# Kernel tuning notes

Hardware: AMD Instinct MI355X
Metric: run time of the kernel (lower is better)

The kernel has to match this reference:

```python
import jax, jax.numpy as jnp
import numpy as np
import math

B, S, E, H, L, C, DFF = 8, 1024, 512, 8, 2, 8921, 2048
DH = E // H
LN_EPS = 1e-5


def _make_pe(max_len, d):
    pos = np.arange(max_len, dtype=np.float32)[:, None]
    div = np.exp(np.arange(0, d, 2, dtype=np.float32) * (-math.log(10000.0) / d))
    pe = np.zeros((max_len, d), dtype=np.float32)
    pe[:, 0::2] = np.sin(pos * div)
    pe[:, 1::2] = np.cos(pos * div)
    return jnp.asarray(pe)


def setup_inputs() -> dict:
    key = jax.random.key(0)
    ks = jax.random.split(key, 16)
    sc = 0.02
    return {
        'inputs': jax.random.normal(ks[0], (B, S, E), jnp.float32),
        'pe': _make_pe(S, E),
        'label_mat': jax.random.normal(ks[1], (C, E), jnp.float32) * sc,
        'l1_w': jax.random.normal(ks[2], (E, E), jnp.float32) * sc,
        'l1_b': jnp.zeros((E,), jnp.float32),
        'fc_w': jax.random.normal(ks[3], (C, E), jnp.float32) * sc,
        'fc_b': jnp.zeros((C,), jnp.float32),
        'in_proj_w': jax.random.normal(ks[4], (L, 3 * E, E), jnp.float32) * sc,
        'in_proj_b': jnp.zeros((L, 3 * E), jnp.float32),
        'out_proj_w': jax.random.normal(ks[5], (L, E, E), jnp.float32) * sc,
        'out_proj_b': jnp.zeros((L, E), jnp.float32),
        'ln1_w': jnp.ones((L, E), jnp.float32),
        'ln1_b': jnp.zeros((L, E), jnp.float32),
        'ln2_w': jnp.ones((L, E), jnp.float32),
        'ln2_b': jnp.zeros((L, E), jnp.float32),
        'lin1_w': jax.random.normal(ks[6], (L, DFF, E), jnp.float32) * sc,
        'lin1_b': jnp.zeros((L, DFF), jnp.float32),
        'lin2_w': jax.random.normal(ks[7], (L, E, DFF), jnp.float32) * sc,
        'lin2_b': jnp.zeros((L, E), jnp.float32),
    }


def _ln(x, g, b):
    mu = jnp.mean(x, axis=-1, keepdims=True)
    v = jnp.mean(jnp.square(x - mu), axis=-1, keepdims=True)
    return (x - mu) * jax.lax.rsqrt(v + LN_EPS) * g + b


def _encoder_layer(x, wqkv, bqkv, wo, bo, g1, b1, g2, b2, w1, bb1, w2, bb2):
    # x: [B,S,E]; post-norm torch TransformerEncoderLayer with relu
    qkv = x @ wqkv.T + bqkv                      # [B,S,3E]
    q, k, v = jnp.split(qkv, 3, axis=-1)
    q = q.reshape(B, S, H, DH)
    k = k.reshape(B, S, H, DH)
    v = v.reshape(B, S, H, DH)
    scores = jnp.einsum('bqhd,bkhd->bhqk', q, k) / math.sqrt(DH)
    attn = jax.nn.softmax(scores, axis=-1)
    o = jnp.einsum('bhqk,bkhd->bqhd', attn, v).reshape(B, S, E)
    o = o @ wo.T + bo
    x = _ln(x + o, g1, b1)
    ff = jax.nn.relu(x @ w1.T + bb1) @ w2.T + bb2
    return _ln(x + ff, g2, b2)


def reference(inputs, pe, label_mat, l1_w, l1_b, fc_w, fc_b,
              in_proj_w, in_proj_b, out_proj_w, out_proj_b,
              ln1_w, ln1_b, ln2_w, ln2_b,
              lin1_w, lin1_b, lin2_w, lin2_b):
    # faithful to source: pe is indexed by batch position (source bug)
    x = inputs * math.sqrt(E) + pe[:B][:, None, :]      # [B,S,E]
    for i in range(L):
        x = _encoder_layer(x, in_proj_w[i], in_proj_b[i], out_proj_w[i], out_proj_b[i],
                           ln1_w[i], ln1_b[i], ln2_w[i], ln2_b[i],
                           lin1_w[i], lin1_b[i], lin2_w[i], lin2_b[i])
    # label attention
    o1 = jnp.tanh(x @ l1_w.T + l1_b)                    # [B,S,E]
    scores = o1 @ label_mat.T                           # [B,S,C]
    attn_weights = jax.nn.softmax(scores, axis=1)       # over seq dim
    attn_weights = jnp.swapaxes(attn_weights, 1, 2)     # [B,C,S]
    weighted = attn_weights @ x                         # [B,C,E]
    # fused per-class linears: C tiny GEMVs -> one einsum
    outputs = jnp.einsum('bce,ce->bc', weighted, fc_w) + fc_b  # [B,C]
    return outputs, attn_weights
```

## Files before the change

### kernel.cpp

```cpp
#include <hip/hip_runtime.h>
#include <math.h>

#define BB   8
#define SS   1024
#define EE   512
#define HH   8
#define DHH  64
#define LLY  2
#define CC   8921
#define CP   9088
#define DFF_ 2048

typedef short          bf16x8 __attribute__((ext_vector_type(8)));
typedef float          f32x4  __attribute__((ext_vector_type(4)));
typedef unsigned short u16x4  __attribute__((ext_vector_type(4)));
typedef unsigned short u16x8  __attribute__((ext_vector_type(8)));

__device__ __forceinline__ float bf2f(unsigned short u) {
    return __uint_as_float(((unsigned int)u) << 16);
}
__device__ __forceinline__ unsigned short f2bf(float f) {
    unsigned int u = __float_as_uint(f);
    u = (u + 0x7FFFu + ((u >> 16) & 1u)) >> 16;
    return (unsigned short)u;
}
__device__ __forceinline__ void gload16(const void* g, void* l) {
    __builtin_amdgcn_global_load_lds(
        (const __attribute__((address_space(1))) void*)g,
        (__attribute__((address_space(3))) void*)l, 16, 0, 0);
}

__global__ __launch_bounds__(256) void cvt_bf16(const float* __restrict__ in,
                                                unsigned short* __restrict__ out,
                                                long n_in, long n_out)
{
    const long i4 = ((long)blockIdx.x * 256 + threadIdx.x) * 4;
    if (i4 >= n_out) return;
    u16x4 r;
    if (i4 < n_in) {
        const float4 v = *(const float4*)(in + i4);
        r[0] = f2bf(v.x); r[1] = f2bf(v.y); r[2] = f2bf(v.z); r[3] = f2bf(v.w);
    } else {
        r[0] = r[1] = r[2] = r[3] = 0;
    }
    *(u16x4*)(out + i4) = r;
}

__global__ __launch_bounds__(256) void embed_kernel(const float* __restrict__ in,
                                                    const float* __restrict__ pe,
                                                    float* __restrict__ x,
                                                    unsigned short* __restrict__ xb)
{
    const long i  = (long)blockIdx.x * 256 + threadIdx.x;
    const int  e4 = (int)(i & 127);
    const int  b  = (int)(i >> 17);
    float4 v = ((const float4*)in)[i];
    const float4 p = ((const float4*)pe)[b * 128 + e4];
    const float sc = 22.627416997969522f;
    v.x = v.x * sc + p.x;  v.y = v.y * sc + p.y;
    v.z = v.z * sc + p.z;  v.w = v.w * sc + p.w;
    ((float4*)x)[i] = v;
    u16x4 h; h[0] = f2bf(v.x); h[1] = f2bf(v.y); h[2] = f2bf(v.z); h[3] = f2bf(v.w);
    ((u16x4*)xb)[i] = h;
}

__global__ __launch_bounds__(256) void gemm_mfma(const unsigned short* __restrict__ A,
                                                 const unsigned short* __restrict__ B,
                                                 const float* __restrict__ bias,
                                                 float* __restrict__ Cf,
                                                 unsigned short* __restrict__ Ch,
                                                 int M, int N, int K, int Mlim,
                                                 long sAz, long sBz, long sCz,
                                                 int act, int mode)
{
    __shared__ unsigned short As[128 * 64];
    __shared__ unsigned short Bs[128 * 64];
    const int t  = threadIdx.x;
    const int wv = t >> 6, ln = t & 63;
    const int wr = wv >> 1, wc = wv & 1;
    const int lr = ln & 15, lg = ln >> 4;
    const int m0 = blockIdx.x * 128, n0 = blockIdx.y * 128;
    const int z  = blockIdx.z;
    const unsigned short* Ab = A + (long)z * sAz;
    const unsigned short* Bb = B + (long)z * sBz;

    const int srow = ln >> 3;
    const int ucol = ((ln & 7) ^ srow) << 3;

    f32x4 acc[4][4];
    #pragma unroll
    for (int i = 0; i < 4; ++i)
        #pragma unroll
        for (int j = 0; j < 4; ++j)
            acc[i][j] = (f32x4){0.f, 0.f, 0.f, 0.f};

    int rA[4], rB[4];
    #pragma unroll
    for (int f = 0; f < 4; ++f) {
        rA[f] = wr * 64 + f * 16 + lr;
        rB[f] = wc * 64 + f * 16 + lr;
    }

    for (int k0 = 0; k0 < K; k0 += 64) {
        __syncthreads();
        #pragma unroll
        for (int c = 0; c < 4; ++c) {
            const int q   = (wv << 2) + c;
            const int row = (q << 3) + srow;
            gload16(Ab + (long)(m0 + row) * K + k0 + ucol, (char*)As + (q << 10));
            gload16(Bb + (long)(n0 + row) * K + k0 + ucol, (char*)Bs + (q << 10));
        }
        __syncthreads();
        #pragma unroll
        for (int kk = 0; kk < 2; ++kk) {
            bf16x8 af[4], bg[4];
            const int s = (kk << 2) + lg;
            #pragma unroll
            for (int f = 0; f < 4; ++f) {
                af[f] = *(const bf16x8*)((const char*)As + rA[f] * 128 + ((s ^ (rA[f] & 7)) << 4));
                bg[f] = *(const bf16x8*)((const char*)Bs + rB[f] * 128 + ((s ^ (rB[f] & 7)) << 4));
            }
            #pragma unroll
            for (int i = 0; i < 4; ++i)
                #pragma unroll
                for (int j = 0; j < 4; ++j)
                    acc[i][j] = __builtin_amdgcn_mfma_f32_16x16x32_bf16(af[i], bg[j], acc[i][j], 0, 0, 0);
        }
    }

    const long zC = (long)z * sCz;
    #pragma unroll
    for (int fm = 0; fm < 4; ++fm) {
        #pragma unroll
        for (int reg = 0; reg < 4; ++reg) {
            const int gm = m0 + wr * 64 + fm * 16 + lg * 4 + reg;
            if (gm >= Mlim) continue;
            #pragma unroll
            for (int fn = 0; fn < 4; ++fn) {
                const int gn = n0 + wc * 64 + fn * 16 + lr;
                float v = acc[fm][fn][reg];
                if (bias) v += bias[gn];
                if (act == 1)      v = fmaxf(v, 0.f);
                else if (act == 2) v = tanhf(v);
                if (mode & 1) Cf[zC + (long)gm * N + gn] = v;
                if (mode & 2) Ch[zC + (long)gm * N + gn] = f2bf(v);
            }
        }
    }
}

__global__ __launch_bounds__(256) void gemm_label_mfma(const unsigned short* __restrict__ A,
                                                       const unsigned short* __restrict__ B,
                                                       const float* __restrict__ attn,
                                                       float* __restrict__ out)
{
    __shared__ unsigned short As[128 * 64];
    __shared__ unsigned short Bs[128 * 64];
    const int t  = threadIdx.x;
    const int wv = t >> 6, ln = t & 63;
    const int wr = wv >> 1, wc = wv & 1;
    const int lr = ln & 15, lg = ln >> 4;
    const int m0 = blockIdx.x * 128, n0 = blockIdx.y * 128;
    const int z  = blockIdx.z;
    const unsigned short* Bb = B + (long)z * SS * EE;

    const int srow = ln >> 3;
    const int ucol = ((ln & 7) ^ srow) << 3;

    f32x4 acc[4][4];
    #pragma unroll
    for (int i = 0; i < 4; ++i)
        #pragma unroll
        for (int j = 0; j < 4; ++j)
            acc[i][j] = (f32x4){0.f, 0.f, 0.f, 0.f};

    int rA[4], rB[4];
    #pragma unroll
    for (int f = 0; f < 4; ++f) {
        rA[f] = wr * 64 + f * 16 + lr;
        rB[f] = wc * 64 + f * 16 + lr;
    }

    for (int k0 = 0; k0 < EE; k0 += 64) {
        __syncthreads();
        #pragma unroll
        for (int c = 0; c < 4; ++c) {
            const int q   = (wv << 2) + c;
            const int row = (q << 3) + srow;
            gload16(A  + (long)(m0 + row) * EE + k0 + ucol, (char*)As + (q << 10));
            gload16(Bb + (long)(n0 + row) * EE + k0 + ucol, (char*)Bs + (q << 10));
        }
        __syncthreads();
        #pragma unroll
        for (int kk = 0; kk < 2; ++kk) {
            bf16x8 af[4], bg[4];
            const int s = (kk << 2) + lg;
            #pragma unroll
            for (int f = 0; f < 4; ++f) {
                af[f] = *(const bf16x8*)((const char*)As + rA[f] * 128 + ((s ^ (rA[f] & 7)) << 4));
                bg[f] = *(const bf16x8*)((const char*)Bs + rB[f] * 128 + ((s ^ (rB[f] & 7)) << 4));
            }
            #pragma unroll
            for (int i = 0; i < 4; ++i)
                #pragma unroll
                for (int j = 0; j < 4; ++j)
                    acc[i][j] = __builtin_amdgcn_mfma_f32_16x16x32_bf16(af[i], bg[j], acc[i][j], 0, 0, 0);
        }
    }

    const float* attb = attn + (long)z * CC * SS;
    float*       outb = out  + (long)z * CC;
    #pragma unroll
    for (int fm = 0; fm < 4; ++fm) {
        #pragma unroll
        for (int reg = 0; reg < 4; ++reg) {
            const int r = m0 + wr * 64 + fm * 16 + lg * 4 + reg;
            float p = 0.f;
            if (r < CC) {
                #pragma unroll
                for (int fn = 0; fn < 4; ++fn) {
                    const int sn = n0 + wc * 64 + fn * 16 + lr;
                    p += acc[fm][fn][reg] * attb[(long)r * SS + sn];
                }
            }
            p += __shfl_xor(p, 1);
            p += __shfl_xor(p, 2);
            p += __shfl_xor(p, 4);
            p += __shfl_xor(p, 8);
            if (lr == 0 && r < CC) atomicAdd(&outb[r], p);
        }
    }
}

__global__ __launch_bounds__(256) void vtrans(const unsigned short* __restrict__ qkv,
                                              unsigned short* __restrict__ Vt)
{
    __shared__ unsigned short tile[64][72];
    const int bh = blockIdx.y, b = bh >> 3, h = bh & 7;
    const int s0 = blockIdx.x << 6;
    const int t  = threadIdx.x;
    const int r  = t >> 3;
    const int c8 = (t & 7) << 3;
    const unsigned short* vb = qkv + (long)b * SS * 1536 + 2 * EE + h * DHH;
    #pragma unroll
    for (int rr = 0; rr < 64; rr += 32)
        *(u16x8*)&tile[r + rr][c8] = *(const u16x8*)(vb + (long)(s0 + r + rr) * 1536 + c8);
    __syncthreads();
    #pragma unroll
    for (int rr = 0; rr < 64; rr += 32) {
        const int d = r + rr;
        u16x8 o;
        #pragma unroll
        for (int j = 0; j < 8; ++j) o[j] = tile[c8 + j][d];
        *(u16x8*)(Vt + ((long)bh * DHH + d) * SS + s0 + c8) = o;
    }
}

__global__ __launch_bounds__(256) void flash_mfma(const unsigned short* __restrict__ qkv,
                                                  const unsigned short* __restrict__ Vt,
                                                  unsigned short* __restrict__ o)
{
    __shared__ unsigned short sP[4][16 * 64];
    const int t  = threadIdx.x;
    const int wv = t >> 6, ln = t & 63;
    const int lr = ln & 15, lg = ln >> 4;
    const int bh = blockIdx.y, b = bh >> 3, h = bh & 7;
    const int q0 = (blockIdx.x << 6) + (wv << 4);

    const unsigned short* qb = qkv + (long)b * SS * 1536 + h * DHH;
    const unsigned short* kb = qb + EE;
    const unsigned short* vt = Vt + (long)bh * DHH * SS;
    unsigned short* pw = sP[wv];

    bf16x8 aq[2];
    #pragma unroll
    for (int c = 0; c < 2; ++c)
        aq[c] = *(const bf16x8*)(qb + (long)(q0 + lr) * 1536 + (c << 5) + (lg << 3));

    float m_[4], l_[4];
    f32x4 accO[4];
    #pragma unroll
    for (int r = 0; r < 4; ++r) { m_[r] = -1e30f; l_[r] = 0.f; }
    #pragma unroll
    for (int n = 0; n < 4; ++n) accO[n] = (f32x4){0.f, 0.f, 0.f, 0.f};

    for (int s0 = 0; s0 < SS; s0 += 64) {
        f32x4 accS[4];
        #pragma unroll
        for (int sj = 0; sj < 4; ++sj) accS[sj] = (f32x4){0.f, 0.f, 0.f, 0.f};
        #pragma unroll
        for (int c = 0; c < 2; ++c) {
            #pragma unroll
            for (int sj = 0; sj < 4; ++sj) {
                const bf16x8 kf = *(const bf16x8*)(kb + (long)(s0 + (sj << 4) + lr) * 1536 + (c << 5) + (lg << 3));
                accS[sj] = __builtin_amdgcn_mfma_f32_16x16x32_bf16(aq[c], kf, accS[sj], 0, 0, 0);
            }
        }
        #pragma unroll
        for (int reg = 0; reg < 4; ++reg) {
            float sc0 = accS[0][reg] * 0.125f, sc1 = accS[1][reg] * 0.125f;
            float sc2 = accS[2][reg] * 0.125f, sc3 = accS[3][reg] * 0.125f;
            float mx = fmaxf(fmaxf(sc0, sc1), fmaxf(sc2, sc3));
            mx = fmaxf(mx, __shfl_xor(mx, 1));
            mx = fmaxf(mx, __shfl_xor(mx, 2));
            mx = fmaxf(mx, __shfl_xor(mx, 4));
            mx = fmaxf(mx, __shfl_xor(mx, 8));
            const float mnew = fmaxf(m_[reg], mx);
            const float f = __expf(m_[reg] - mnew);
            m_[reg] = mnew;
            sc0 = __expf(sc0 - mnew); sc1 = __expf(sc1 - mnew);
            sc2 = __expf(sc2 - mnew); sc3 = __expf(sc3 - mnew);
            accS[0][reg] = sc0; accS[1][reg] = sc1;
            accS[2][reg] = sc2; accS[3][reg] = sc3;
            float ss = sc0 + sc1 + sc2 + sc3;
            ss += __shfl_xor(ss, 1); ss += __shfl_xor(ss, 2);
            ss += __shfl_xor(ss, 4); ss += __shfl_xor(ss, 8);
            l_[reg] = l_[reg] * f + ss;
            #pragma unroll
            for (int n = 0; n < 4; ++n) accO[n][reg] *= f;
        }
        #pragma unroll
        for (int sj = 0; sj < 4; ++sj) {
            #pragma unroll
            for (int reg = 0; reg < 4; ++reg) {
                const int q = (lg << 2) + reg;
                const int s = (sj << 4) + lr;
                const int byte = (q << 7) + (((s >> 3) ^ (q & 7)) << 4) + ((s & 7) << 1);
                *(unsigned short*)((char*)pw + byte) = f2bf(accS[sj][reg]);
            }
        }
        #pragma unroll
        for (int c2 = 0; c2 < 2; ++c2) {
            const int slot = ((c2 << 2) + lg) ^ (lr & 7);
            const bf16x8 pa = *(const bf16x8*)((const char*)pw + (lr << 7) + (slot << 4));
            #pragma unroll
            for (int n = 0; n < 4; ++n) {
                const bf16x8 vf = *(const bf16x8*)(vt + (long)((n << 4) + lr) * SS + s0 + (c2 << 5) + (lg << 3));
                accO[n] = __builtin_amdgcn_mfma_f32_16x16x32_bf16(pa, vf, accO[n], 0, 0, 0);
            }
        }
    }

    #pragma unroll
    for (int reg = 0; reg < 4; ++reg) {
        const float inv = 1.f / l_[reg];
        unsigned short* orow = o + (long)(b * SS + q0 + (lg << 2) + reg) * EE + h * DHH;
        #pragma unroll
        for (int n = 0; n < 4; ++n)
            orow[(n << 4) + lr] = f2bf(accO[n][reg] * inv);
    }
}

__global__ __launch_bounds__(256) void ln_fused(float* __restrict__ x,
                                                unsigned short* __restrict__ xb,
                                                const float* __restrict__ o,
                                                const float* __restrict__ g,
                                                const float* __restrict__ bta)
{
    const long row = blockIdx.x;
    float* xr = x + row * EE;
    unsigned short* hb = xb + row * EE;
    const float* orr = o + row * EE;
    const int t = threadIdx.x;
    const float v0 = xr[t] + orr[t];
    const float v1 = xr[t + 256] + orr[t + 256];
    float s = v0 + v1;
    #pragma unroll
    for (int off = 1; off < 64; off <<= 1) s += __shfl_xor(s, off);
    __shared__ float r1[4], r2[4];
    if ((t & 63) == 0) r1[t >> 6] = s;
    __syncthreads();
    const float mu = (r1[0] + r1[1] + r1[2] + r1[3]) * (1.f / EE);
    const float d0 = v0 - mu, d1 = v1 - mu;
    float q = d0 * d0 + d1 * d1;
    #pragma unroll
    for (int off = 1; off < 64; off <<= 1) q += __shfl_xor(q, off);
    if ((t & 63) == 0) r2[t >> 6] = q;
    __syncthreads();
    const float rs = rsqrtf((r2[0] + r2[1] + r2[2] + r2[3]) * (1.f / EE) + 1e-5f);
    const float y0 = d0 * rs * g[t]       + bta[t];
    const float y1 = d1 * rs * g[t + 256] + bta[t + 256];
    xr[t] = y0;  xr[t + 256] = y1;
    hb[t] = f2bf(y0);  hb[t + 256] = f2bf(y1);
}

__global__ __launch_bounds__(256) void label_softmax(float* __restrict__ attn)
{
    const long row = blockIdx.x;
    float* p = attn + row * (long)SS;
    const int t = threadIdx.x;
    float4 v = ((float4*)p)[t];
    __shared__ float red[4];
    float mx = fmaxf(fmaxf(v.x, v.y), fmaxf(v.z, v.w));
    #pragma unroll
    for (int off = 1; off < 64; off <<= 1) mx = fmaxf(mx, __shfl_xor(mx, off));
    if ((t & 63) == 0) red[t >> 6] = mx;
    __syncthreads();
    mx = fmaxf(fmaxf(red[0], red[1]), fmaxf(red[2], red[3]));
    v.x = __expf(v.x - mx); v.y = __expf(v.y - mx);
    v.z = __expf(v.z - mx); v.w = __expf(v.w - mx);
    float s = v.x + v.y + v.z + v.w;
    #pragma unroll
    for (int off = 1; off < 64; off <<= 1) s += __shfl_xor(s, off);
    __syncthreads();
    if ((t & 63) == 0) red[t >> 6] = s;
    __syncthreads();
    const float inv = 1.f / (red[0] + red[1] + red[2] + red[3]);
    v.x *= inv; v.y *= inv; v.z *= inv; v.w *= inv;
    ((float4*)p)[t] = v;
}

__global__ __launch_bounds__(256) void init_out(float* __restrict__ out,
                                                const float* __restrict__ fcb)
{
    const int i = blockIdx.x * 256 + threadIdx.x;
    if (i < BB * CC) out[i] = fcb[i % CC];
}

extern "C" void kernel_launch(void* const* d_in, const int* in_sizes, int n_in,
                              void* d_out, int out_size, void* d_ws, size_t ws_size,
                              hipStream_t stream)
{
    const float* inp   = (const float*)d_in[0];
    const float* pe    = (const float*)d_in[1];
    const float* label = (const float*)d_in[2];
    const float* l1w   = (const float*)d_in[3];
    const float* l1b   = (const float*)d_in[4];
    const float* fcw   = (const float*)d_in[5];
    const float* fcb   = (const float*)d_in[6];
    const float* ipw   = (const float*)d_in[7];
    const float* ipb   = (const float*)d_in[8];
    const float* opw   = (const float*)d_in[9];
    const float* opb   = (const float*)d_in[10];
    const float* g1    = (const float*)d_in[11];
    const float* b1    = (const float*)d_in[12];
    const float* g2    = (const float*)d_in[13];
    const float* b2    = (const float*)d_in[14];
    const float* w1    = (const float*)d_in[15];
    const float* bb1   = (const float*)d_in[16];
    const float* w2    = (const float*)d_in[17];
    const float* bb2   = (const float*)d_in[18];

    char* wp = (char*)d_ws;
    float* x = (float*)wp;                 wp += (long)BB * SS * EE * 4;
    unsigned short* xb = (unsigned short*)wp;  wp += (long)BB * SS * EE * 2;
    float* bufo = (float*)wp;              wp += (long)BB * SS * EE * 4;
    unsigned short* big = (unsigned short*)wp; wp += (long)BB * SS * DFF_ * 2;
    unsigned short* ob  = (unsigned short*)wp; wp += (long)BB * SS * EE * 2;
    unsigned short* Vtb = (unsigned short*)wp; wp += (long)BB * HH * DHH * SS * 2;
    unsigned short* ipwb = (unsigned short*)wp; wp += (long)LLY * 3 * EE * EE * 2;
    unsigned short* opwb = (unsigned short*)wp; wp += (long)LLY * EE * EE * 2;
    unsigned short* w1b  = (unsigned short*)wp; wp += (long)LLY * DFF_ * EE * 2;
    unsigned short* w2b  = (unsigned short*)wp; wp += (long)LLY * EE * DFF_ * 2;
    unsigned short* l1wb = (unsigned short*)wp; wp += (long)EE * EE * 2;
    unsigned short* labelb = (unsigned short*)wp; wp += (long)CP * EE * 2;
    unsigned short* fcwb   = (unsigned short*)wp; wp += (long)CP * EE * 2;

    float* out0  = (float*)d_out;
    float* attnW = out0 + BB * CC;

    {
        const long n1 = (long)LLY * 3 * EE * EE;
        cvt_bf16<<<(int)((n1 / 4 + 255) / 256), 256, 0, stream>>>(ipw, ipwb, n1, n1);
        const long n2 = (long)LLY * EE * EE;
        cvt_bf16<<<(int)((n2 / 4 + 255) / 256), 256, 0, stream>>>(opw, opwb, n2, n2);
        const long n3 = (long)LLY * DFF_ * EE;
        cvt_bf16<<<(int)((n3 / 4 + 255) / 256), 256, 0, stream>>>(w1, w1b, n3, n3);
        cvt_bf16<<<(int)((n3 / 4 + 255) / 256), 256, 0, stream>>>(w2, w2b, n3, n3);
        const long n4 = (long)EE * EE;
        cvt_bf16<<<(int)((n4 / 4 + 255) / 256), 256, 0, stream>>>(l1w, l1wb, n4, n4);
        const long n5i = (long)CC * EE, n5o = (long)CP * EE;
        cvt_bf16<<<(int)((n5o / 4 + 255) / 256), 256, 0, stream>>>(label, labelb, n5i, n5o);
        cvt_bf16<<<(int)((n5o / 4 + 255) / 256), 256, 0, stream>>>(fcw, fcwb, n5i, n5o);
    }

    const int M = BB * SS;

    embed_kernel<<<4096, 256, 0, stream>>>(inp, pe, x, xb);

    for (int l = 0; l < LLY; ++l) {
        gemm_mfma<<<dim3(64, 12, 1), 256, 0, stream>>>(xb, ipwb + (long)l * 3 * EE * EE,
                                                       ipb + l * 3 * EE, nullptr, big,
                                                       M, 3 * EE, EE, M, 0, 0, 0, 0, 2);
        vtrans<<<dim3(16, 64), 256, 0, stream>>>(big, Vtb);
        flash_mfma<<<dim3(16, 64), 256, 0, stream>>>(big, Vtb, ob);
        gemm_mfma<<<dim3(64, 4, 1), 256, 0, stream>>>(ob, opwb + (long)l * EE * EE,
                                                      opb + l * EE, bufo, nullptr,
                                                      M, EE, EE, M, 0, 0, 0, 0, 1);
        ln_fused<<<M, 256, 0, stream>>>(x, xb, bufo, g1 + l * EE, b1 + l * EE);
        gemm_mfma<<<dim3(64, 16, 1), 256, 0, stream>>>(xb, w1b + (long)l * DFF_ * EE,
                                                       bb1 + l * DFF_, nullptr, big,
                                                       M, DFF_, EE, M, 0, 0, 0, 1, 2);
        gemm_mfma<<<dim3(64, 4, 1), 256, 0, stream>>>(big, w2b + (long)l * EE * DFF_,
                                                      bb2 + l * EE, bufo, nullptr,
                                                      M, EE, DFF_, M, 0, 0, 0, 0, 1);
        ln_fused<<<M, 256, 0, stream>>>(x, xb, bufo, g2 + l * EE, b2 + l * EE);
    }

    gemm_mfma<<<dim3(64, 4, 1), 256, 0, stream>>>(xb, l1wb, l1b, nullptr, ob,
                                                  M, EE, EE, M, 0, 0, 0, 2, 2);
    gemm_mfma<<<dim3(CP / 128, SS / 128, BB), 256, 0, stream>>>(labelb, ob, nullptr, attnW, nullptr,
                                                                CP, SS, EE, CC,
                                                                0, (long)SS * EE, (long)CC * SS, 0, 1);
    label_softmax<<<BB * CC, 256, 0, stream>>>(attnW);
    init_out<<<(BB * CC + 255) / 256, 256, 0, stream>>>(out0, fcb);
    gemm_label_mfma<<<dim3(CP / 128, SS / 128, BB), 256, 0, stream>>>(fcwb, xb, attnW, out0);
}
```

Measured before the change: 1.232 ms.

## Fuse label softmax into score and final GEMMs; stage K/V in LDS for flash

The label-score GEMM now writes raw scores and also emits per-tile partial softmax statistics (max and sum of exponentials). A small merge kernel combines these into per-row max and inverse sum. The final fc GEMM then normalises the scores in its epilogue, writes the probabilities back and accumulates the output. This removes the standalone softmax pass over the large B×C×S attention tensor. Separately, flash attention now stages K and V tiles in swizzled LDS shared by all four waves, instead of each wave reading them from global memory, at the cost of two barriers per tile.

```diff
diff --git a/kernel.cpp b/kernel.cpp
--- a/kernel.cpp
+++ b/kernel.cpp
@@ -149,10 +149,10 @@
     }
 }
 
-__global__ __launch_bounds__(256) void gemm_label_mfma(const unsigned short* __restrict__ A,
-                                                       const unsigned short* __restrict__ B,
-                                                       const float* __restrict__ attn,
-                                                       float* __restrict__ out)
+__global__ __launch_bounds__(256) void gemm_scores(const unsigned short* __restrict__ A,
+                                                   const unsigned short* __restrict__ B,
+                                                   float* __restrict__ attnW,
+                                                   float2* __restrict__ stats)
 {
     __shared__ unsigned short As[128 * 64];
     __shared__ unsigned short Bs[128 * 64];
@@ -208,26 +208,137 @@
         }
     }
 
-    const float* attb = attn + (long)z * CC * SS;
-    float*       outb = out  + (long)z * CC;
+    float* aw = attnW + (long)z * CC * SS;
     #pragma unroll
     for (int fm = 0; fm < 4; ++fm) {
         #pragma unroll
         for (int reg = 0; reg < 4; ++reg) {
             const int r = m0 + wr * 64 + fm * 16 + lg * 4 + reg;
-            float p = 0.f;
+            float v0 = acc[fm][0][reg], v1 = acc[fm][1][reg];
+            float v2 = acc[fm][2][reg], v3 = acc[fm][3][reg];
             if (r < CC) {
                 #pragma unroll
                 for (int fn = 0; fn < 4; ++fn) {
                     const int sn = n0 + wc * 64 + fn * 16 + lr;
-                    p += acc[fm][fn][reg] * attb[(long)r * SS + sn];
+                    aw[(long)r * SS + sn] = acc[fm][fn][reg];
                 }
             }
-            p += __shfl_xor(p, 1);
-            p += __shfl_xor(p, 2);
-            p += __shfl_xor(p, 4);
-            p += __shfl_xor(p, 8);
-            if (lr == 0 && r < CC) atomicAdd(&outb[r], p);
+            float mx = fmaxf(fmaxf(v0, v1), fmaxf(v2, v3));
+            mx = fmaxf(mx, __shfl_xor(mx, 1));
+            mx = fmaxf(mx, __shfl_xor(mx, 2));
+            mx = fmaxf(mx, __shfl_xor(mx, 4));
+            mx = fmaxf(mx, __shfl_xor(mx, 8));
+            float sm = __expf(v0 - mx) + __expf(v1 - mx) + __expf(v2 - mx) + __expf(v3 - mx);
+            sm += __shfl_xor(sm, 1); sm += __shfl_xor(sm, 2);
+            sm += __shfl_xor(sm, 4); sm += __shfl_xor(sm, 8);
+            if (lr == 0 && r < CC)
+                stats[((long)z * CP + r) * 16 + blockIdx.y * 2 + wc] = make_float2(mx, sm);
+        }
+    }
+}
+
+__global__ __launch_bounds__(256) void merge_stats(const float2* __restrict__ stats,
+                                                   float2* __restrict__ rowstat)
+{
+    const long idx = (long)blockIdx.x * 256 + threadIdx.x;
+    if (idx >= (long)BB * CP) return;
+    const int c = (int)(idx % CP);
+    if (c >= CC) return;
+    const float2* s = stats + idx * 16;
+    float mx = -1e30f;
+    #pragma unroll
+    for (int i = 0; i < 16; ++i) mx = fmaxf(mx, s[i].x);
+    float tot = 0.f;
+    #pragma unroll
+    for (int i = 0; i < 16; ++i) tot += s[i].y * __expf(s[i].x - mx);
+    rowstat[idx] = make_float2(mx, 1.f / tot);
+}
+
+__global__ __launch_bounds__(256) void gemm_label_final(const unsigned short* __restrict__ A,
+                                                        const unsigned short* __restrict__ B,
+                                                        float* __restrict__ attnW,
+                                                        const float2* __restrict__ rowstat,
+                                                        float* __restrict__ out)
+{
+    __shared__ unsigned short As[128 * 64];
+    __shared__ unsigned short Bs[128 * 64];
+    const int t  = threadIdx.x;
+    const int wv = t >> 6, ln = t & 63;
+    const int wr = wv >> 1, wc = wv & 1;
+    const int lr = ln & 15, lg = ln >> 4;
+    const int m0 = blockIdx.x * 128, n0 = blockIdx.y * 128;
+    const int z  = blockIdx.z;
+    const unsigned short* Bb = B + (long)z * SS * EE;
+
+    const int srow = ln >> 3;
+    const int ucol = ((ln & 7) ^ srow) << 3;
+
+    f32x4 acc[4][4];
+    #pragma unroll
+    for (int i = 0; i < 4; ++i)
+        #pragma unroll
+        for (int j = 0; j < 4; ++j)
+            acc[i][j] = (f32x4){0.f, 0.f, 0.f, 0.f};
+
+    int rA[4], rB[4];
+    #pragma unroll
+    for (int f = 0; f < 4; ++f) {
+        rA[f] = wr * 64 + f * 16 + lr;
+        rB[f] = wc * 64 + f * 16 + lr;
+    }
+
+    for (int k0 = 0; k0 < EE; k0 += 64) {
+        __syncthreads();
+        #pragma unroll
+        for (int c = 0; c < 4; ++c) {
+            const int q   = (wv << 2) + c;
+            const int row = (q << 3) + srow;
+            gload16(A  + (long)(m0 + row) * EE + k0 + ucol, (char*)As + (q << 10));
+            gload16(Bb + (long)(n0 + row) * EE + k0 + ucol, (char*)Bs + (q << 10));
+        }
+        __syncthreads();
+        #pragma unroll
+        for (int kk = 0; kk < 2; ++kk) {
+            bf16x8 af[4], bg[4];
+            const int s = (kk << 2) + lg;
+            #pragma unroll
+            for (int f = 0; f < 4; ++f) {
+                af[f] = *(const bf16x8*)((const char*)As + rA[f] * 128 + ((s ^ (rA[f] & 7)) << 4));
+                bg[f] = *(const bf16x8*)((const char*)Bs + rB[f] * 128 + ((s ^ (rB[f] & 7)) << 4));
+            }
+            #pragma unroll
+            for (int i = 0; i < 4; ++i)
+                #pragma unroll
+                for (int j = 0; j < 4; ++j)
+                    acc[i][j] = __builtin_amdgcn_mfma_f32_16x16x32_bf16(af[i], bg[j], acc[i][j], 0, 0, 0);
+        }
+    }
+
+    float* aw = attnW + (long)z * CC * SS;
+    const float2* rs = rowstat + (long)z * CP;
+    float* outb = out + (long)z * CC;
+    #pragma unroll
+    for (int fm = 0; fm < 4; ++fm) {
+        #pragma unroll
+        for (int reg = 0; reg < 4; ++reg) {
+            const int r = m0 + wr * 64 + fm * 16 + lg * 4 + reg;
+            float pacc = 0.f;
+            if (r < CC) {
+                const float2 st = rs[r];
+                #pragma unroll
+                for (int fn = 0; fn < 4; ++fn) {
+                    const int sn = n0 + wc * 64 + fn * 16 + lr;
+                    const float raw = aw[(long)r * SS + sn];
+                    const float p = __expf(raw - st.x) * st.y;
+                    aw[(long)r * SS + sn] = p;
+                    pacc += p * acc[fm][fn][reg];
+                }
+            }
+            pacc += __shfl_xor(pacc, 1);
+            pacc += __shfl_xor(pacc, 2);
+            pacc += __shfl_xor(pacc, 4);
+            pacc += __shfl_xor(pacc, 8);
+            if (lr == 0 && r < CC) atomicAdd(&outb[r], pacc);
         }
     }
 }
@@ -260,6 +371,8 @@
                                                   const unsigned short* __restrict__ Vt,
                                                   unsigned short* __restrict__ o)
 {
+    __shared__ unsigned short sK[64 * 64];
+    __shared__ unsigned short sV[64 * 64];
     __shared__ unsigned short sP[4][16 * 64];
     const int t  = threadIdx.x;
     const int wv = t >> 6, ln = t & 63;
@@ -272,6 +385,9 @@
     const unsigned short* vt = Vt + (long)bh * DHH * SS;
     unsigned short* pw = sP[wv];
 
+    const int srow = ln >> 3;
+    const int ucol = ((ln & 7) ^ srow) << 3;
+
     bf16x8 aq[2];
     #pragma unroll
     for (int c = 0; c < 2; ++c)
@@ -285,14 +401,25 @@
     for (int n = 0; n < 4; ++n) accO[n] = (f32x4){0.f, 0.f, 0.f, 0.f};
 
     for (int s0 = 0; s0 < SS; s0 += 64) {
+        __syncthreads();
+        #pragma unroll
+        for (int c = 0; c < 2; ++c) {
+            const int row = (wv << 4) + (c << 3) + srow;
+            gload16(kb + (long)(s0 + row) * 1536 + ucol, (char*)sK + (((wv << 1) + c) << 10));
+            gload16(vt + (long)row * SS + s0 + ucol,     (char*)sV + (((wv << 1) + c) << 10));
+        }
+        __syncthreads();
+
         f32x4 accS[4];
         #pragma unroll
         for (int sj = 0; sj < 4; ++sj) accS[sj] = (f32x4){0.f, 0.f, 0.f, 0.f};
         #pragma unroll
         for (int c = 0; c < 2; ++c) {
+            const int slot = (c << 2) + lg;
             #pragma unroll
             for (int sj = 0; sj < 4; ++sj) {
-                const bf16x8 kf = *(const bf16x8*)(kb + (long)(s0 + (sj << 4) + lr) * 1536 + (c << 5) + (lg << 3));
+                const int rw = (sj << 4) + lr;
+                const bf16x8 kf = *(const bf16x8*)((const char*)sK + rw * 128 + ((slot ^ (rw & 7)) << 4));
                 accS[sj] = __builtin_amdgcn_mfma_f32_16x16x32_bf16(aq[c], kf, accS[sj], 0, 0, 0);
             }
         }
@@ -331,11 +458,13 @@
         }
         #pragma unroll
         for (int c2 = 0; c2 < 2; ++c2) {
-            const int slot = ((c2 << 2) + lg) ^ (lr & 7);
-            const bf16x8 pa = *(const bf16x8*)((const char*)pw + (lr << 7) + (slot << 4));
+            const int pslot = ((c2 << 2) + lg) ^ (lr & 7);
+            const bf16x8 pa = *(const bf16x8*)((const char*)pw + (lr << 7) + (pslot << 4));
+            const int vslot = (c2 << 2) + lg;
             #pragma unroll
             for (int n = 0; n < 4; ++n) {
-                const bf16x8 vf = *(const bf16x8*)(vt + (long)((n << 4) + lr) * SS + s0 + (c2 << 5) + (lg << 3));
+                const int rw = (n << 4) + lr;
+                const bf16x8 vf = *(const bf16x8*)((const char*)sV + rw * 128 + ((vslot ^ (rw & 7)) << 4));
                 accO[n] = __builtin_amdgcn_mfma_f32_16x16x32_bf16(pa, vf, accO[n], 0, 0, 0);
             }
         }
@@ -382,32 +511,6 @@
     const float y1 = d1 * rs * g[t + 256] + bta[t + 256];
     xr[t] = y0;  xr[t + 256] = y1;
     hb[t] = f2bf(y0);  hb[t + 256] = f2bf(y1);
-}
-
-__global__ __launch_bounds__(256) void label_softmax(float* __restrict__ attn)
-{
-    const long row = blockIdx.x;
-    float* p = attn + row * (long)SS;
-    const int t = threadIdx.x;
-    float4 v = ((float4*)p)[t];
-    __shared__ float red[4];
-    float mx = fmaxf(fmaxf(v.x, v.y), fmaxf(v.z, v.w));
-    #pragma unroll
-    for (int off = 1; off < 64; off <<= 1) mx = fmaxf(mx, __shfl_xor(mx, off));
-    if ((t & 63) == 0) red[t >> 6] = mx;
-    __syncthreads();
-    mx = fmaxf(fmaxf(red[0], red[1]), fmaxf(red[2], red[3]));
-    v.x = __expf(v.x - mx); v.y = __expf(v.y - mx);
-    v.z = __expf(v.z - mx); v.w = __expf(v.w - mx);
-    float s = v.x + v.y + v.z + v.w;
-    #pragma unroll
-    for (int off = 1; off < 64; off <<= 1) s += __shfl_xor(s, off);
-    __syncthreads();
-    if ((t & 63) == 0) red[t >> 6] = s;
-    __syncthreads();
-    const float inv = 1.f / (red[0] + red[1] + red[2] + red[3]);
-    v.x *= inv; v.y *= inv; v.z *= inv; v.w *= inv;
-    ((float4*)p)[t] = v;
 }
 
 __global__ __launch_bounds__(256) void init_out(float* __restrict__ out,
@@ -455,6 +558,8 @@
     unsigned short* l1wb = (unsigned short*)wp; wp += (long)EE * EE * 2;
     unsigned short* labelb = (unsigned short*)wp; wp += (long)CP * EE * 2;
     unsigned short* fcwb   = (unsigned short*)wp; wp += (long)CP * EE * 2;
+    float2* stats   = (float2*)wp;         wp += (long)BB * CP * 16 * 8;
+    float2* rowstat = (float2*)wp;         wp += (long)BB * CP * 8;
 
     float* out0  = (float*)d_out;
     float* attnW = out0 + BB * CC;
@@ -499,10 +604,8 @@
 
     gemm_mfma<<<dim3(64, 4, 1), 256, 0, stream>>>(xb, l1wb, l1b, nullptr, ob,
                                                   M, EE, EE, M, 0, 0, 0, 2, 2);
-    gemm_mfma<<<dim3(CP / 128, SS / 128, BB), 256, 0, stream>>>(labelb, ob, nullptr, attnW, nullptr,
-                                                                CP, SS, EE, CC,
-                                                                0, (long)SS * EE, (long)CC * SS, 0, 1);
-    label_softmax<<<BB * CC, 256, 0, stream>>>(attnW);
+    gemm_scores<<<dim3(CP / 128, SS / 128, BB), 256, 0, stream>>>(labelb, ob, attnW, stats);
+    merge_stats<<<(int)(((long)BB * CP + 255) / 256), 256, 0, stream>>>(stats, rowstat);
     init_out<<<(BB * CC + 255) / 256, 256, 0, stream>>>(out0, fcb);
-    gemm_label_mfma<<<dim3(CP / 128, SS / 128, BB), 256, 0, stream>>>(fcwb, xb, attnW, out0);
-}
+    gemm_label_final<<<dim3(CP / 128, SS / 128, BB), 256, 0, stream>>>(fcwb, xb, attnW, rowstat, out0);
+}
```

After: 1.100 ms. -10.7%, faster.
